# Optimization experiments

Measured on AMD Instinct MI355X. Metric: run time of the kernel, lower is better.

## Reference

```python
import jax, jax.numpy as jnp
import numpy as np

B, S, E, R = 128, 16, 512, 1000
_SCALE = np.float32(1.0 / np.sqrt(E))


def setup_inputs() -> dict:
    key = jax.random.key(0)
    ks = jax.random.split(key, 12)
    s = 1.0 / np.sqrt(E)
    u = lambda k, shape: jax.random.uniform(k, shape, jnp.float32, -s, s)
    emb = jax.random.normal(ks[0], (R + 1, E), jnp.float32).at[R].set(0.0)  # padding_idx row = 0
    return {
        "tokens": jax.random.randint(ks[11], (B, S), 0, R),
        "emb": emb,
        "W_ih": u(ks[1], (3 * E, E)), "W_hh": u(ks[2], (3 * E, E)),
        "b_ih": u(ks[3], (3 * E,)), "b_hh": u(ks[4], (3 * E,)),
        "w_fc": u(ks[5], (E,)), "b_fc": u(ks[6], ()),
        "Wq": u(ks[7], (E, E)), "bq": u(ks[8], (E,)),
        "Wk": u(ks[9], (E, E)), "bk": u(ks[10], (E,)),
    }


def _gru_step(x, h, W_ih, W_hh, b_ih, b_hh):
    # torch GRU cell: gates stacked as [r; z; n]
    gi = x @ W_ih.T + b_ih
    gh = h @ W_hh.T + b_hh
    ir, iz, inn = jnp.split(gi, 3, axis=-1)
    hr, hz, hn = jnp.split(gh, 3, axis=-1)
    r = jax.nn.sigmoid(ir + hr)
    z = jax.nn.sigmoid(iz + hz)
    n = jnp.tanh(inn + r * hn)
    return (1.0 - z) * n + z * h


def _attention(x, emb, Wq, bq, Wk, bk):
    # x: [B,1,E]; key = fc_k(cat(relation_emb, x)); scores = q k^T / sqrt(E)
    Bn = x.shape[0]
    rel = jnp.broadcast_to(emb[:R][None], (Bn, R, E))
    all_emb = jnp.concatenate([rel, x], axis=1)        # [B,R+1,E]
    q = x @ Wq.T + bq
    k = all_emb @ Wk.T + bk
    scores = jnp.einsum('bqe,bke->bqk', q, k) * _SCALE  # [B,1,R+1]
    return scores, all_emb


def _entropy(scores):
    lp = jax.nn.log_softmax(scores, axis=-1)
    return -jnp.sum(jnp.exp(lp) * lp, axis=-1)          # [B,1]


def _reduce(x, emb, W_ih, W_hh, b_ih, b_hh, w_fc, b_fc, Wq, bq, Wk, bk):
    Bn, L, Ed = x.shape
    if L > 2:
        # vectorized 2-step GRU over all adjacent pairs (replaces python while loop)
        h1 = _gru_step(x[:, :-1], jnp.zeros_like(x[:, :-1]), W_ih, W_hh, b_ih, b_hh)
        pairs = _gru_step(x[:, 1:], h1, W_ih, W_hh, b_ih, b_hh)   # [B,L-1,E]
        score = jax.nn.sigmoid(pairs @ w_fc + b_fc)               # [B,L-1]
        sel = jnp.argmax(score, axis=-1)                          # [B]
        barange = jnp.arange(Bn)
        pair = pairs[barange, sel][:, None]                       # [B,1,E]
        scores, all_emb = _attention(pair, emb, Wq, bq, Wk, bk)
        loss = _entropy(scores)
        prob = jax.nn.softmax(scores, axis=-1)                    # weightedAverage mask is all-False for seq_len=1
        merged = jnp.einsum('bqk,bke->bqe', prob, all_emb)[:, 0]  # [B,E]
        # output = inputs.detach().clone(); overwrite sel with merged; delete row sel+1
        out = jax.lax.stop_gradient(x).at[barange, sel].set(merged)
        j = jnp.arange(L - 1)[None]
        src = j + (j >= (sel + 1)[:, None])                       # skip zeroed row sel+1
        out = out[barange[:, None], src]                          # [B,L-1,E]
        return out, loss
    else:
        h1 = _gru_step(x[:, 0], jnp.zeros_like(x[:, 0]), W_ih, W_hh, b_ih, b_hh)
        h2 = _gru_step(x[:, 1], h1, W_ih, W_hh, b_ih, b_hh)
        return h2[:, None], jnp.zeros((Bn, 1), x.dtype)


def reference(tokens, emb, W_ih, W_hh, b_ih, b_hh, w_fc, b_fc, Wq, bq, Wk, bk):
    x = emb[tokens]                                               # [B,S,E]
    losses = []
    for _ in range(tokens.shape[1] - 1):
        x, l = _reduce(x, emb, W_ih, W_hh, b_ih, b_hh, w_fc, b_fc, Wq, bq, Wk, bk)
        losses.append(l)
    scores, _ = _attention(x, emb, Wq, bq, Wk, bk)                # x is [B,1,E]
    losses.append(_entropy(scores))
    return scores[:, 0], jnp.concatenate(losses, axis=-1)         # ([B,R+1], [B,S])
```

## Files before the change

### kernel.cpp

```cpp
#include <hip/hip_runtime.h>

#define B 128
#define S 16
#define E 512
#define R 1000
#define K3 1536
#define NW0 1920
#define NWS 256
#define NS (B * (R + 1))
#define SCALE 0.04419417382415922f

static __device__ __forceinline__ float sigm(float x) { return 1.f / (1.f + expf(-x)); }

static __device__ __forceinline__ float brsum(float v, float* sb) {
  int tid = threadIdx.x;
  sb[tid] = v; __syncthreads();
  for (int s = 128; s > 0; s >>= 1) {
    if (tid < s) sb[tid] += sb[tid + s];
    __syncthreads();
  }
  float r = sb[0]; __syncthreads();
  return r;
}
static __device__ __forceinline__ float brmax(float v, float* sb) {
  int tid = threadIdx.x;
  sb[tid] = v; __syncthreads();
  for (int s = 128; s > 0; s >>= 1) {
    if (tid < s) sb[tid] = fmaxf(sb[tid], sb[tid + s]);
    __syncthreads();
  }
  float r = sb[0]; __syncthreads();
  return r;
}
static __device__ __forceinline__ void brsum2(float v1, float v2, float* sb, float* sb2,
                                              float* o1, float* o2) {
  int tid = threadIdx.x;
  sb[tid] = v1; sb2[tid] = v2; __syncthreads();
  for (int s = 128; s > 0; s >>= 1) {
    if (tid < s) { sb[tid] += sb[tid + s]; sb2[tid] += sb2[tid + s]; }
    __syncthreads();
  }
  *o1 = sb[0]; *o2 = sb2[0]; __syncthreads();
}

#define TILE_FMA \
  _Pragma("unroll") \
  for (int k = 0; k < 16; ++k) { \
    float4 a4 = *(const float4*)&As[k][ty * 4]; \
    float4 w4 = *(const float4*)&Ws[k][tx * 4]; \
    acc[0][0] = fmaf(a4.x, w4.x, acc[0][0]); acc[0][1] = fmaf(a4.x, w4.y, acc[0][1]); \
    acc[0][2] = fmaf(a4.x, w4.z, acc[0][2]); acc[0][3] = fmaf(a4.x, w4.w, acc[0][3]); \
    acc[1][0] = fmaf(a4.y, w4.x, acc[1][0]); acc[1][1] = fmaf(a4.y, w4.y, acc[1][1]); \
    acc[1][2] = fmaf(a4.y, w4.z, acc[1][2]); acc[1][3] = fmaf(a4.y, w4.w, acc[1][3]); \
    acc[2][0] = fmaf(a4.z, w4.x, acc[2][0]); acc[2][1] = fmaf(a4.z, w4.y, acc[2][1]); \
    acc[2][2] = fmaf(a4.z, w4.z, acc[2][2]); acc[2][3] = fmaf(a4.z, w4.w, acc[2][3]); \
    acc[3][0] = fmaf(a4.w, w4.x, acc[3][0]); acc[3][1] = fmaf(a4.w, w4.y, acc[3][1]); \
    acc[3][2] = fmaf(a4.w, w4.z, acc[3][2]); acc[3][3] = fmaf(a4.w, w4.w, acc[3][3]); \
  }

#define TILE_FMA32 \
  _Pragma("unroll") \
  for (int k = 0; k < 16; ++k) { \
    float2 a2 = *(const float2*)&As[k][ty * 2]; \
    float4 w4 = *(const float4*)&Ws[k][tx * 4]; \
    acc[0][0] = fmaf(a2.x, w4.x, acc[0][0]); acc[0][1] = fmaf(a2.x, w4.y, acc[0][1]); \
    acc[0][2] = fmaf(a2.x, w4.z, acc[0][2]); acc[0][3] = fmaf(a2.x, w4.w, acc[0][3]); \
    acc[1][0] = fmaf(a2.y, w4.x, acc[1][0]); acc[1][1] = fmaf(a2.y, w4.y, acc[1][1]); \
    acc[1][2] = fmaf(a2.y, w4.z, acc[1][2]); acc[1][3] = fmaf(a2.y, w4.w, acc[1][3]); \
  }

__global__ __launch_bounds__(256) void k_gemm(const float* __restrict__ A, int lda, int M,
                                              const float* __restrict__ W, int N, int K,
                                              const float* __restrict__ bias, float scale,
                                              float* __restrict__ C, int ldc) {
  __shared__ float As[16][64];
  __shared__ float Ws[16][64];
  int tid = threadIdx.x;
  int mBase = blockIdx.y * 64;
  int nBase = blockIdx.x * 64;
  int tx = tid & 15, ty = tid >> 4;
  int li = tid & 63;
  int lk = (tid >> 6) * 4;
  float acc[4][4] = {{0.f,0.f,0.f,0.f},{0.f,0.f,0.f,0.f},{0.f,0.f,0.f,0.f},{0.f,0.f,0.f,0.f}};
  int m = mBase + li;
  const float* Arow = (m < M) ? (A + (size_t)m * lda) : nullptr;
  int n = nBase + li;
  const float* Wrow = (n < N) ? (W + (size_t)n * K) : nullptr;

  float4 av = Arow ? *(const float4*)(Arow + lk) : make_float4(0.f, 0.f, 0.f, 0.f);
  float4 wv = Wrow ? *(const float4*)(Wrow + lk) : make_float4(0.f, 0.f, 0.f, 0.f);

  for (int k0 = 0; k0 < K; k0 += 16) {
    As[lk + 0][li] = av.x; As[lk + 1][li] = av.y;
    As[lk + 2][li] = av.z; As[lk + 3][li] = av.w;
    Ws[lk + 0][li] = wv.x; Ws[lk + 1][li] = wv.y;
    Ws[lk + 2][li] = wv.z; Ws[lk + 3][li] = wv.w;
    __syncthreads();
    if (k0 + 16 < K) {
      av = Arow ? *(const float4*)(Arow + k0 + 16 + lk) : make_float4(0.f, 0.f, 0.f, 0.f);
      wv = Wrow ? *(const float4*)(Wrow + k0 + 16 + lk) : make_float4(0.f, 0.f, 0.f, 0.f);
    }
    TILE_FMA
    __syncthreads();
  }
#pragma unroll
  for (int r = 0; r < 4; ++r) {
    int mm = mBase + ty * 4 + r;
    if (mm >= M) continue;
#pragma unroll
    for (int c = 0; c < 4; ++c) {
      int nn = nBase + tx * 4 + c;
      if (nn >= N) continue;
      float v = acc[r][c] * scale;
      if (bias) v += bias[nn];
      C[(size_t)mm * ldc + nn] = v;
    }
  }
}

__global__ __launch_bounds__(256) void k_gemmD(const float* __restrict__ A, int lda, int M,
                                               const float* __restrict__ W1, int N1,
                                               const float* __restrict__ b1,
                                               float* __restrict__ C1, int ldc1,
                                               const float* __restrict__ W2, int N2,
                                               float* __restrict__ C2, int ldc2, int K) {
  __shared__ float As[16][64];
  __shared__ float Ws[16][64];
  int tid = threadIdx.x;
  int mBase = blockIdx.y * 64;
  int nBase = blockIdx.x * 64;
  int tx = tid & 15, ty = tid >> 4;
  int li = tid & 63;
  int lk = (tid >> 6) * 4;
  float acc[4][4] = {{0.f,0.f,0.f,0.f},{0.f,0.f,0.f,0.f},{0.f,0.f,0.f,0.f},{0.f,0.f,0.f,0.f}};
  int m = mBase + li;
  const float* Arow = (m < M) ? (A + (size_t)m * lda) : nullptr;
  int n = nBase + li;
  const float* Wrow = nullptr;
  if (n < N1) Wrow = W1 + (size_t)n * K;
  else if (n < N1 + N2) Wrow = W2 + (size_t)(n - N1) * K;

  float4 av = Arow ? *(const float4*)(Arow + lk) : make_float4(0.f, 0.f, 0.f, 0.f);
  float4 wv = Wrow ? *(const float4*)(Wrow + lk) : make_float4(0.f, 0.f, 0.f, 0.f);

  for (int k0 = 0; k0 < K; k0 += 16) {
    As[lk + 0][li] = av.x; As[lk + 1][li] = av.y;
    As[lk + 2][li] = av.z; As[lk + 3][li] = av.w;
    Ws[lk + 0][li] = wv.x; Ws[lk + 1][li] = wv.y;
    Ws[lk + 2][li] = wv.z; Ws[lk + 3][li] = wv.w;
    __syncthreads();
    if (k0 + 16 < K) {
      av = Arow ? *(const float4*)(Arow + k0 + 16 + lk) : make_float4(0.f, 0.f, 0.f, 0.f);
      wv = Wrow ? *(const float4*)(Wrow + k0 + 16 + lk) : make_float4(0.f, 0.f, 0.f, 0.f);
    }
    TILE_FMA
    __syncthreads();
  }
#pragma unroll
  for (int r = 0; r < 4; ++r) {
    int mm = mBase + ty * 4 + r;
    if (mm >= M) continue;
#pragma unroll
    for (int c = 0; c < 4; ++c) {
      int nn = nBase + tx * 4 + c;
      if (nn < N1) {
        float v = acc[r][c];
        if (b1) v += b1[nn];
        C1[(size_t)mm * ldc1 + nn] = v;
      } else if (nn < N1 + N2) {
        C2[(size_t)mm * ldc2 + (nn - N1)] = acc[r][c];
      }
    }
  }
}

static __device__ void dev_g64(float (*As)[64], float (*Ws)[64], int tid,
                               int mBase, int nBase,
                               const float* __restrict__ A, int lda, int M,
                               const float* __restrict__ W, int N, int K,
                               const float* __restrict__ bias, float scale,
                               float* __restrict__ C, int ldc) {
  int tx = tid & 15, ty = tid >> 4;
  int li = tid & 63;
  int lk = (tid >> 6) * 4;
  float acc[4][4] = {{0.f,0.f,0.f,0.f},{0.f,0.f,0.f,0.f},{0.f,0.f,0.f,0.f},{0.f,0.f,0.f,0.f}};
  int m = mBase + li;
  const float* Arow = (m < M) ? (A + (size_t)m * lda) : nullptr;
  int n = nBase + li;
  const float* Wrow = (n < N) ? (W + (size_t)n * K) : nullptr;

  float4 av = Arow ? *(const float4*)(Arow + lk) : make_float4(0.f, 0.f, 0.f, 0.f);
  float4 wv = Wrow ? *(const float4*)(Wrow + lk) : make_float4(0.f, 0.f, 0.f, 0.f);

  for (int k0 = 0; k0 < K; k0 += 16) {
    As[lk + 0][li] = av.x; As[lk + 1][li] = av.y;
    As[lk + 2][li] = av.z; As[lk + 3][li] = av.w;
    Ws[lk + 0][li] = wv.x; Ws[lk + 1][li] = wv.y;
    Ws[lk + 2][li] = wv.z; Ws[lk + 3][li] = wv.w;
    __syncthreads();
    if (k0 + 16 < K) {
      av = Arow ? *(const float4*)(Arow + k0 + 16 + lk) : make_float4(0.f, 0.f, 0.f, 0.f);
      wv = Wrow ? *(const float4*)(Wrow + k0 + 16 + lk) : make_float4(0.f, 0.f, 0.f, 0.f);
    }
    TILE_FMA
    __syncthreads();
  }
#pragma unroll
  for (int r = 0; r < 4; ++r) {
    int mm = mBase + ty * 4 + r;
    if (mm >= M) continue;
#pragma unroll
    for (int c = 0; c < 4; ++c) {
      int nn = nBase + tx * 4 + c;
      if (nn >= N) continue;
      float v = acc[r][c] * scale;
      if (bias) v += bias[nn];
      C[(size_t)mm * ldc + nn] = v;
    }
  }
}

static __device__ void dev_tr64(float (*t)[65], int tid, const float* __restrict__ src,
                                int Cc, float* __restrict__ dst, int ldd, int bx, int by) {
  int tx = tid & 15, ty = tid >> 4;
  int rb = by * 64, cb = bx * 64;
#pragma unroll
  for (int i = 0; i < 4; ++i) {
    int r = rb + ty + i * 16;
    float4 v = *(const float4*)(src + (size_t)r * Cc + cb + tx * 4);
    t[ty + i * 16][tx * 4 + 0] = v.x; t[ty + i * 16][tx * 4 + 1] = v.y;
    t[ty + i * 16][tx * 4 + 2] = v.z; t[ty + i * 16][tx * 4 + 3] = v.w;
  }
  __syncthreads();
#pragma unroll
  for (int i = 0; i < 4; ++i) {
    int c = cb + ty + i * 16;
    float4 v;
    v.x = t[tx * 4 + 0][ty + i * 16]; v.y = t[tx * 4 + 1][ty + i * 16];
    v.z = t[tx * 4 + 2][ty + i * 16]; v.w = t[tx * 4 + 3][ty + i * 16];
    *(float4*)(dst + (size_t)c * ldd + rb + tx * 4) = v;
  }
}

__global__ __launch_bounds__(256) void k_prep(const float* __restrict__ Wq,
                                              const float* __restrict__ Wk,
                                              const float* __restrict__ Wih,
                                              float* __restrict__ WqT,
                                              float* __restrict__ WkT,
                                              float* __restrict__ Wbig,
                                              int* __restrict__ pos,
                                              int* __restrict__ wlb,
                                              int* __restrict__ wlL,
                                              int* __restrict__ wlR,
                                              float* __restrict__ outp) {
  __shared__ float t[64][65];
  int blk = blockIdx.x, tid = threadIdx.x;
  if (blk < 64) {
    dev_tr64(t, tid, Wq, E, WqT, E, blk & 7, blk >> 3);
  } else if (blk < 128) {
    int j = blk - 64;
    dev_tr64(t, tid, Wk, E, WkT, E, j & 7, j >> 3);
  } else if (blk < 320) {
    int j = blk - 128;
    dev_tr64(t, tid, Wih, E, Wbig + (size_t)1024 * K3, K3, j & 7, j >> 3);
  } else if (blk < 328) {
    int idx = (blk - 320) * 256 + tid;
    if (idx < B * 16) pos[idx] = idx & 15;
    if (idx < NW0) {
      wlb[idx] = idx / 15;
      int i = idx % 15;
      wlL[idx] = i;
      wlR[idx] = i + 1;
    }
    if (idx < B) outp[NS + idx * 16 + 14] = 0.f;
  } else {
    int idx = (blk - 328) * 256 + tid;
    for (int i = idx; i < 24 * K3; i += 8 * 256) Wbig[(size_t)1000 * K3 + i] = 0.f;
  }
}

__global__ __launch_bounds__(256) void k_setup3(const float* __restrict__ KREL,
                                                const float* __restrict__ WqT,
                                                const float* __restrict__ WkT,
                                                const float* __restrict__ bq,
                                                const float* __restrict__ bk,
                                                float* __restrict__ Gbig,
                                                float* __restrict__ v12,
                                                float* __restrict__ c0s,
                                                float* __restrict__ gb) {
  __shared__ float As[16][64];
  __shared__ float Ws[16][64];
  int blk = blockIdx.x, tid = threadIdx.x;
  if (blk < 128) {
    dev_g64(As, Ws, tid, (blk >> 3) * 64, (blk & 7) * 64, KREL, E, R, WqT, E, E,
            nullptr, 1.f, Gbig, E);
  } else if (blk < 192) {
    int j = blk - 128;
    dev_g64(As, Ws, tid, (j >> 3) * 64, (j & 7) * 64, WqT, E, E, WkT, E, E,
            nullptr, 1.f, Gbig + (size_t)1000 * E, E);
  } else {
    int m = blk - 192;
    if (m < 2) {
      int i = m * 256 + tid;
      const float* wq = WqT + (size_t)i * E;
      const float* wk = WkT + (size_t)i * E;
      float s = 0.f;
      for (int e = 0; e < E; ++e) s += wq[e] * bk[e] + bq[e] * wk[e];
      v12[i] = s;
    } else if (m == 2) {
      float* sb = (float*)As;
      float p = 0.f;
      for (int e = tid; e < E; e += 256) p += bq[e] * bk[e];
      float s = brsum(p, sb);
      if (tid == 0) c0s[0] = s;
    } else {
      int r = (m - 3) * 256 + tid;
      if (r < R) {
        const float* kr = KREL + (size_t)r * E;
        float s = 0.f;
        for (int e = 0; e < E; ++e) s += bq[e] * kr[e];
        gb[r] = s;
      }
    }
  }
}

__global__ __launch_bounds__(256) void k_giinit(const int* __restrict__ tokens,
                                                const float* __restrict__ Wbig,
                                                const float* __restrict__ bih,
                                                float* __restrict__ GI,
                                                const float* __restrict__ gb,
                                                float* __restrict__ SCT,
                                                const float* __restrict__ bhh,
                                                float* __restrict__ H1C) {
  int row = blockIdx.x, tid = threadIdx.x;
  if (row < B * S) {
    int tok = tokens[row];
    const float4* src = (const float4*)(Wbig + (size_t)tok * K3);
    const float4* bv = (const float4*)bih;
    float* girow = GI + (size_t)row * K3;
    float4* dst = (float4*)girow;
    for (int i = tid; i < K3 / 4; i += 256) {
      float4 a = src[i], b = bv[i];
      dst[i] = make_float4(a.x + b.x, a.y + b.y, a.z + b.z, a.w + b.w);
    }
    int i16 = row & 15;
    if (i16 < 15) {
      __syncthreads();
      float* h = H1C + (size_t)((row >> 4) * 15 + i16) * E;
      for (int e = tid; e < E; e += 256) {
        float r = sigm(girow[e] + bhh[e]);
        float z = sigm(girow[E + e] + bhh[E + e]);
        h[e] = (1.f - z) * tanhf(girow[2 * E + e] + r * bhh[2 * E + e]);
      }
    }
  } else {
    int rb = row - B * S;
    for (int m = rb * 16; m < rb * 16 + 16; ++m) {
      float* r = SCT + (size_t)m * K3;
      for (int n = tid; n < 1512; n += 256) r[n] = (n < 1000) ? gb[n] : 0.f;
    }
  }
}

__global__ __launch_bounds__(256) void k_h1c(const int* __restrict__ wlb,
                                             const int* __restrict__ wlL,
                                             const float* __restrict__ GI,
                                             const float* __restrict__ bhh,
                                             float* __restrict__ H1C,
                                             float* __restrict__ GHC) {
  int w = blockIdx.x, tid = threadIdx.x;
  const float* gi = GI + (size_t)(wlb[w] * 16 + wlL[w]) * K3;
  float* h = H1C + (size_t)w * E;
  for (int e = tid; e < E; e += 256) {
    float r = sigm(gi[e] + bhh[e]);
    float z = sigm(gi[E + e] + bhh[E + e]);
    h[e] = (1.f - z) * tanhf(gi[2 * E + e] + r * bhh[2 * E + e]);
  }
  if (GHC) {
    float* g = GHC + (size_t)w * K3;
    for (int n = tid; n < K3; n += 256) g[n] = bhh[n];
  }
}

__global__ __launch_bounds__(256) void k_ghcs(const float* __restrict__ H1C,
                                              const float* __restrict__ Whh,
                                              float* __restrict__ GHC) {
  __shared__ float As[16][32];
  __shared__ float Ws[16][64];
  int tid = threadIdx.x;
  int nBase = blockIdx.x * 64;
  int mBase = blockIdx.y * 32;
  int kbeg = blockIdx.z * 256;
  int tx = tid & 15, ty = tid >> 4;
  int ar = tid & 31, ak = (tid >> 5) * 2;
  int li = tid & 63, lk = (tid >> 6) * 4;
  float acc[2][4] = {{0.f,0.f,0.f,0.f},{0.f,0.f,0.f,0.f}};
  const float* Arow = H1C + (size_t)(mBase + ar) * E + kbeg;
  const float* Wrow = Whh + (size_t)(nBase + li) * E + kbeg;
  float2 av = *(const float2*)(Arow + ak);
  float4 wv = *(const float4*)(Wrow + lk);
  for (int k0 = 0; k0 < 256; k0 += 16) {
    As[ak + 0][ar] = av.x; As[ak + 1][ar] = av.y;
    Ws[lk + 0][li] = wv.x; Ws[lk + 1][li] = wv.y;
    Ws[lk + 2][li] = wv.z; Ws[lk + 3][li] = wv.w;
    __syncthreads();
    if (k0 + 16 < 256) {
      av = *(const float2*)(Arow + k0 + 16 + ak);
      wv = *(const float4*)(Wrow + k0 + 16 + lk);
    }
    TILE_FMA32
    __syncthreads();
  }
#pragma unroll
  for (int r = 0; r < 2; ++r) {
    int mm = mBase + ty * 2 + r;
#pragma unroll
    for (int c = 0; c < 4; ++c) {
      int nn = nBase + tx * 4 + c;
      atomicAdd(&GHC[(size_t)mm * K3 + nn], acc[r][c]);
    }
  }
}

__global__ __launch_bounds__(256) void k_pairc(const int* __restrict__ wlb,
                                               const int* __restrict__ wlL,
                                               const int* __restrict__ wlR,
                                               const float* __restrict__ GI,
                                               const float* __restrict__ GHC,
                                               const float* __restrict__ H1C,
                                               const float* __restrict__ wfc,
                                               const float* __restrict__ bfc,
                                               float* __restrict__ PAIR,
                                               float* __restrict__ SCR) {
  __shared__ float sb[256];
  int w = blockIdx.x, tid = threadIdx.x;
  int b = wlb[w], ls = wlL[w], rs = wlR[w];
  const float* gr = GI + (size_t)(b * 16 + rs) * K3;
  const float* gh = GHC + (size_t)w * K3;
  const float* h = H1C + (size_t)w * E;
  float* p = PAIR + (size_t)(b * 16 + ls) * E;
  float part = 0.f;
  for (int e = tid; e < E; e += 256) {
    float r = sigm(gr[e] + gh[e]);
    float z = sigm(gr[E + e] + gh[E + e]);
    float n = tanhf(gr[2 * E + e] + r * gh[2 * E + e]);
    float pv = (1.f - z) * n + z * h[e];
    p[e] = pv;
    part += pv * wfc[e];
  }
  float d = brsum(part, sb);
  if (tid == 0) SCR[b * 16 + ls] = sigm(d + bfc[0]);
}

__global__ __launch_bounds__(256) void k_qscsel(const float* __restrict__ PAIR,
                                                const float* __restrict__ SCR,
                                                const int* __restrict__ pin,
                                                int* __restrict__ pout,
                                                int* __restrict__ wlb,
                                                int* __restrict__ wlL,
                                                int* __restrict__ wlR,
                                                int* __restrict__ xdst,
                                                const float* __restrict__ Gbig,
                                                float* __restrict__ SCT,
                                                float* __restrict__ GI,
                                                const float* __restrict__ bih,
                                                int P, int finalMode) {
  __shared__ float As[16][32];
  __shared__ float Ws[16][64];
  __shared__ int sxd[32];
  int tid = threadIdx.x;
  int nBase = blockIdx.x * 64;
  int mBase = blockIdx.y * 32;
  int kbeg = blockIdx.z * 256;
  if (tid < 32) {
    int b = mBase + tid;
    if (finalMode) {
      int xr = b * 16 + pin[b * 16];
      sxd[tid] = xr;
      if (blockIdx.x == 0 && blockIdx.z == 0) xdst[b] = xr;
    } else {
      int L = P + 1;
      int lp[16];
      for (int i = 0; i < L; ++i) lp[i] = pin[b * 16 + i];
      float best = -1e30f; int sel = 0;
      for (int i = 0; i < P; ++i) {
        float v = SCR[b * 16 + lp[i]];
        if (v > best) { best = v; sel = i; }
      }
      int r1i = (sel + 2 < L) ? sel + 2 : L - 1;
      int l1 = lp[sel], r1 = lp[r1i];
      int l0 = (sel > 0) ? lp[sel - 1] : l1;
      int r0 = (sel > 0) ? lp[sel] : r1;
      sxd[tid] = b * 16 + l1;
      if (blockIdx.x == 0 && blockIdx.z == 0) {
        wlb[2 * b] = b;     wlL[2 * b] = l0;     wlR[2 * b] = r0;
        wlb[2 * b + 1] = b; wlL[2 * b + 1] = l1; wlR[2 * b + 1] = r1;
        xdst[b] = b * 16 + l1;
        for (int i = 0; i < L - 1; ++i)
          pout[b * 16 + i] = (i <= sel) ? lp[i] : lp[i + 1];
      }
    }
  }
  __syncthreads();
  if (!finalMode && blockIdx.z == 1 && blockIdx.x < 16) {
#pragma unroll
    for (int r = 0; r < 2; ++r) {
      float* g = GI + (size_t)sxd[blockIdx.x * 2 + r] * K3;
      for (int i = tid; i < K3; i += 256) g[i] = bih[i];
    }
  }
  int tx = tid & 15, ty = tid >> 4;
  int ar = tid & 31, ak = (tid >> 5) * 2;
  int li = tid & 63, lk = (tid >> 6) * 4;
  float acc[2][4] = {{0.f,0.f,0.f,0.f},{0.f,0.f,0.f,0.f}};
  const float* Arow = PAIR + (size_t)sxd[ar] * E + kbeg;
  int n = nBase + li;
  const float* Wrow = (n < 1512) ? (Gbig + (size_t)n * E + kbeg) : nullptr;
  float2 av = *(const float2*)(Arow + ak);
  float4 wv = Wrow ? *(const float4*)(Wrow + lk) : make_float4(0.f, 0.f, 0.f, 0.f);
  for (int k0 = 0; k0 < 256; k0 += 16) {
    As[ak + 0][ar] = av.x; As[ak + 1][ar] = av.y;
    Ws[lk + 0][li] = wv.x; Ws[lk + 1][li] = wv.y;
    Ws[lk + 2][li] = wv.z; Ws[lk + 3][li] = wv.w;
    __syncthreads();
    if (k0 + 16 < 256) {
      av = *(const float2*)(Arow + k0 + 16 + ak);
      wv = Wrow ? *(const float4*)(Wrow + k0 + 16 + lk) : make_float4(0.f, 0.f, 0.f, 0.f);
    }
    TILE_FMA32
    __syncthreads();
  }
#pragma unroll
  for (int r = 0; r < 2; ++r) {
    int mm = mBase + ty * 2 + r;
#pragma unroll
    for (int c = 0; c < 4; ++c) {
      int nn = nBase + tx * 4 + c;
      if (nn < 1512) atomicAdd(&SCT[(size_t)mm * K3 + nn], acc[r][c]);
    }
  }
}

__global__ __launch_bounds__(256) void k_sm(float* __restrict__ SCT,
                                            const float* __restrict__ PAIR,
                                            const int* __restrict__ xdst,
                                            const float* __restrict__ v12,
                                            const float* __restrict__ c0s,
                                            float* __restrict__ outp,
                                            float* __restrict__ A2,
                                            const float* __restrict__ gb,
                                            int t, int finalMode) {
  __shared__ float sb[256];
  __shared__ float sb2[256];
  __shared__ float sps[E];
  int b = blockIdx.x, tid = threadIdx.x;
  float* row = SCT + (size_t)b * K3;
  int xr = xdst[b];
  const float* sp = PAIR + (size_t)xr * E;
  for (int i = tid; i < E; i += 256) sps[i] = sp[i];
  __syncthreads();
  float part = 0.f;
  for (int i = tid; i < E; i += 256) part += sps[i] * (row[1000 + i] + v12[i]);
  float last = (brsum(part, sb) + c0s[0]) * SCALE;
  float s[4];
  float ml = last;
#pragma unroll
  for (int q = 0; q < 4; ++q) {
    int j = tid + q * 256;
    s[q] = (j < 1000) ? row[j] * SCALE : -1e30f;
    ml = fmaxf(ml, s[q]);
  }
  float mx = brmax(ml, sb);
  float zp = 0.f, s1p = 0.f;
#pragma unroll
  for (int q = 0; q < 4; ++q) {
    int j = tid + q * 256;
    if (j < 1000) { float e = expf(s[q] - mx); zp += e; s1p += e * s[q]; }
  }
  if (tid == 0) { float e = expf(last - mx); zp += e; s1p += e * last; }
  float z, s1;
  brsum2(zp, s1p, sb, sb2, &z, &s1);
  if (tid == 0) outp[NS + b * 16 + t] = mx + logf(z) - s1 / z;
  if (!finalMode) {
    float inv = 1.f / z;
    float* a = A2 + (size_t)b * K3;
#pragma unroll
    for (int q = 0; q < 4; ++q) {
      int j = tid + q * 256;
      if (j < 1000) a[j] = expf(s[q] - mx) * inv;
    }
    if (tid < 24) a[1000 + tid] = 0.f;
    float pr = expf(last - mx) * inv;
    for (int i = tid; i < E; i += 256) a[1024 + i] = pr * sps[i];
    for (int n2 = tid; n2 < 1512; n2 += 256) row[n2] = (n2 < 1000) ? gb[n2] : 0.f;
  } else {
    float* so = outp + (size_t)b * (R + 1);
#pragma unroll
    for (int q = 0; q < 4; ++q) {
      int j = tid + q * 256;
      if (j < 1000) so[j] = s[q];
    }
    if (tid == 0) so[R] = last;
  }
}

__global__ __launch_bounds__(256) void k_giup(const float* __restrict__ A2,
                                              const float* __restrict__ Wbig,
                                              float* __restrict__ GI,
                                              const int* __restrict__ xdst) {
  __shared__ float As[16][32];
  __shared__ float Ws[16][64];
  int tid = threadIdx.x;
  int nBase = blockIdx.x * 64;
  int mBase = blockIdx.y * 32;
  int kbeg = blockIdx.z * 384;
  int tx = tid & 15, ty = tid >> 4;
  int ar = tid & 31, ak = (tid >> 5) * 2;
  int li = tid & 63, wr = tid >> 6;
  float acc[2][4] = {{0.f,0.f,0.f,0.f},{0.f,0.f,0.f,0.f}};
  const float* Arow = A2 + (size_t)(mBase + ar) * K3;
  for (int k0 = kbeg; k0 < kbeg + 384; k0 += 16) {
    float2 av = *(const float2*)(Arow + k0 + ak);
    As[ak + 0][ar] = av.x; As[ak + 1][ar] = av.y;
#pragma unroll
    for (int j = 0; j < 4; ++j)
      Ws[wr * 4 + j][li] = Wbig[(size_t)(k0 + wr * 4 + j) * K3 + nBase + li];
    __syncthreads();
    TILE_FMA32
    __syncthreads();
  }
#pragma unroll
  for (int r = 0; r < 2; ++r) {
    int mm = mBase + ty * 2 + r;
    size_t crow = (size_t)xdst[mm] * K3;
#pragma unroll
    for (int c = 0; c < 4; ++c) {
      int nn = nBase + tx * 4 + c;
      atomicAdd(&GI[crow + nn], acc[r][c]);
    }
  }
}

extern "C" void kernel_launch(void* const* d_in, const int* in_sizes, int n_in,
                              void* d_out, int out_size, void* d_ws, size_t ws_size,
                              hipStream_t stream) {
  (void)in_sizes; (void)n_in; (void)out_size; (void)ws_size;
  const int* tokens = (const int*)d_in[0];
  const float* emb = (const float*)d_in[1];
  const float* W_ih = (const float*)d_in[2];
  const float* W_hh = (const float*)d_in[3];
  const float* b_ih = (const float*)d_in[4];
  const float* b_hh = (const float*)d_in[5];
  const float* w_fc = (const float*)d_in[6];
  const float* b_fc = (const float*)d_in[7];
  const float* Wq = (const float*)d_in[8];
  const float* bq = (const float*)d_in[9];
  const float* Wk = (const float*)d_in[10];
  const float* bk = (const float*)d_in[11];
  float* out = (float*)d_out;

  float* ws = (float*)d_ws;
  size_t o = 0;
  float* GI = ws + o;    o += (size_t)B * S * K3;
  float* GHC = ws + o;   o += (size_t)NW0 * K3;
  float* H1C = ws + o;   o += (size_t)NW0 * E;
  float* PAIR = ws + o;  o += (size_t)B * S * E;
  float* Wbig = ws + o;  o += (size_t)K3 * K3;
  float* Gbig = ws + o;  o += (size_t)1512 * E;
  float* KREL = ws + o;  o += (size_t)R * E;
  float* WqT = ws + o;   o += (size_t)E * E;
  float* WkT = ws + o;   o += (size_t)E * E;
  float* SCT = ws + o;   o += (size_t)B * K3;
  float* A2 = ws + o;    o += (size_t)B * K3;
  float* gb = ws + o;    o += 1024;
  float* v12 = ws + o;   o += 512;
  float* c0s = ws + o;   o += 16;
  float* SCR = ws + o;   o += B * 16;
  int* pos0 = (int*)(ws + o); o += B * 16;
  int* pos1 = (int*)(ws + o); o += B * 16;
  int* wlb = (int*)(ws + o);  o += NW0;
  int* wlL = (int*)(ws + o);  o += NW0;
  int* wlR = (int*)(ws + o);  o += NW0;
  int* xdst = (int*)(ws + o); o += B;

  k_prep<<<336, 256, 0, stream>>>(Wq, Wk, W_ih, WqT, WkT, Wbig, pos0, wlb, wlL, wlR, out);
  k_gemmD<<<dim3(32, 16), 256, 0, stream>>>(emb, E, R, Wk, E, bk, KREL, E,
                                            W_ih, K3, Wbig, K3, E);
  k_setup3<<<199, 256, 0, stream>>>(KREL, WqT, WkT, bq, bk, Gbig, v12, c0s, gb);
  k_giinit<<<B * S + 8, 256, 0, stream>>>(tokens, Wbig, b_ih, GI, gb, SCT, b_hh, H1C);
  k_gemm<<<dim3(24, 30), 256, 0, stream>>>(H1C, E, NW0, W_hh, K3, E, b_hh, 1.f, GHC, K3);
  k_pairc<<<NW0, 256, 0, stream>>>(wlb, wlL, wlR, GI, GHC, H1C, w_fc, b_fc, PAIR, SCR);

  for (int t = 0; t < 14; ++t) {
    int* pin = (t & 1) ? pos1 : pos0;
    int* pout = (t & 1) ? pos0 : pos1;
    k_qscsel<<<dim3(24, 4, 2), 256, 0, stream>>>(PAIR, SCR, pin, pout, wlb, wlL, wlR,
                                                 xdst, Gbig, SCT, GI, b_ih, 15 - t, 0);
    k_sm<<<B, 256, 0, stream>>>(SCT, PAIR, xdst, v12, c0s, out, A2, gb, t, 0);
    k_giup<<<dim3(24, 4, 4), 256, 0, stream>>>(A2, Wbig, GI, xdst);
    k_h1c<<<NWS, 256, 0, stream>>>(wlb, wlL, GI, b_hh, H1C, GHC);
    k_ghcs<<<dim3(24, 8, 2), 256, 0, stream>>>(H1C, W_hh, GHC);
    k_pairc<<<NWS, 256, 0, stream>>>(wlb, wlL, wlR, GI, GHC, H1C, w_fc, b_fc, PAIR, SCR);
  }

  k_qscsel<<<dim3(24, 4, 2), 256, 0, stream>>>(PAIR, SCR, pos0, pos1, wlb, wlL, wlR,
                                               xdst, Gbig, SCT, GI, b_ih, 1, 1);
  k_sm<<<B, 256, 0, stream>>>(SCT, PAIR, xdst, v12, c0s, out, A2, gb, 15, 1);
}
```

Measured before the change: 1.450 ms.

## Cache GRU first-step state per position and recompute only merged rows

The first-step hidden state and its W_hh product are now stored per token position instead of per worklist pair entry. Each iteration recomputes only the one merged position per batch (B rows) rather than every affected pair (NWS rows), which halves the ghcs grid. The GI-init kernel is fused into the setup kernel, and the gb bias is added inside k_sm instead of being pre-filled into SCT. This trades slightly larger workspace buffers and an indirect row lookup for less recompute and one fewer launch.

Result: faster. 1.358 ms (-6.3%).

```diff
diff --git a/kernel.cpp b/kernel.cpp
--- a/kernel.cpp
+++ b/kernel.cpp
@@ -287,7 +287,14 @@
                                                 float* __restrict__ Gbig,
                                                 float* __restrict__ v12,
                                                 float* __restrict__ c0s,
-                                                float* __restrict__ gb) {
+                                                float* __restrict__ gb,
+                                                const int* __restrict__ tokens,
+                                                const float* __restrict__ Wbig,
+                                                const float* __restrict__ bih,
+                                                const float* __restrict__ bhh,
+                                                float* __restrict__ GI,
+                                                float* __restrict__ H1P,
+                                                float* __restrict__ SCT) {
   __shared__ float As[16][64];
   __shared__ float Ws[16][64];
   int blk = blockIdx.x, tid = threadIdx.x;
@@ -298,7 +305,7 @@
     int j = blk - 128;
     dev_g64(As, Ws, tid, (j >> 3) * 64, (j & 7) * 64, WqT, E, E, WkT, E, E,
             nullptr, 1.f, Gbig + (size_t)1000 * E, E);
-  } else {
+  } else if (blk < 199) {
     int m = blk - 192;
     if (m < 2) {
       int i = m * 256 + tid;
@@ -322,19 +329,8 @@
         gb[r] = s;
       }
     }
-  }
-}
-
-__global__ __launch_bounds__(256) void k_giinit(const int* __restrict__ tokens,
-                                                const float* __restrict__ Wbig,
-                                                const float* __restrict__ bih,
-                                                float* __restrict__ GI,
-                                                const float* __restrict__ gb,
-                                                float* __restrict__ SCT,
-                                                const float* __restrict__ bhh,
-                                                float* __restrict__ H1C) {
-  int row = blockIdx.x, tid = threadIdx.x;
-  if (row < B * S) {
+  } else if (blk < 199 + B * S) {
+    int row = blk - 199;
     int tok = tokens[row];
     const float4* src = (const float4*)(Wbig + (size_t)tok * K3);
     const float4* bv = (const float4*)bih;
@@ -344,59 +340,57 @@
       float4 a = src[i], b = bv[i];
       dst[i] = make_float4(a.x + b.x, a.y + b.y, a.z + b.z, a.w + b.w);
     }
-    int i16 = row & 15;
-    if (i16 < 15) {
-      __syncthreads();
-      float* h = H1C + (size_t)((row >> 4) * 15 + i16) * E;
-      for (int e = tid; e < E; e += 256) {
-        float r = sigm(girow[e] + bhh[e]);
-        float z = sigm(girow[E + e] + bhh[E + e]);
-        h[e] = (1.f - z) * tanhf(girow[2 * E + e] + r * bhh[2 * E + e]);
-      }
+    __syncthreads();
+    float* h = H1P + (size_t)row * E;
+    for (int e = tid; e < E; e += 256) {
+      float r = sigm(girow[e] + bhh[e]);
+      float z = sigm(girow[E + e] + bhh[E + e]);
+      h[e] = (1.f - z) * tanhf(girow[2 * E + e] + r * bhh[2 * E + e]);
     }
   } else {
-    int rb = row - B * S;
+    int rb = blk - (199 + B * S);
     for (int m = rb * 16; m < rb * 16 + 16; ++m) {
       float* r = SCT + (size_t)m * K3;
-      for (int n = tid; n < 1512; n += 256) r[n] = (n < 1000) ? gb[n] : 0.f;
-    }
-  }
-}
-
-__global__ __launch_bounds__(256) void k_h1c(const int* __restrict__ wlb,
-                                             const int* __restrict__ wlL,
+      for (int n = tid; n < 1512; n += 256) r[n] = 0.f;
+    }
+  }
+}
+
+__global__ __launch_bounds__(256) void k_h1c(const int* __restrict__ xdst,
                                              const float* __restrict__ GI,
                                              const float* __restrict__ bhh,
-                                             float* __restrict__ H1C,
-                                             float* __restrict__ GHC) {
-  int w = blockIdx.x, tid = threadIdx.x;
-  const float* gi = GI + (size_t)(wlb[w] * 16 + wlL[w]) * K3;
-  float* h = H1C + (size_t)w * E;
+                                             float* __restrict__ H1P,
+                                             float* __restrict__ GHCP) {
+  int p = xdst[blockIdx.x], tid = threadIdx.x;
+  const float* gi = GI + (size_t)p * K3;
+  float* h = H1P + (size_t)p * E;
   for (int e = tid; e < E; e += 256) {
     float r = sigm(gi[e] + bhh[e]);
     float z = sigm(gi[E + e] + bhh[E + e]);
     h[e] = (1.f - z) * tanhf(gi[2 * E + e] + r * bhh[2 * E + e]);
   }
-  if (GHC) {
-    float* g = GHC + (size_t)w * K3;
-    for (int n = tid; n < K3; n += 256) g[n] = bhh[n];
-  }
-}
-
-__global__ __launch_bounds__(256) void k_ghcs(const float* __restrict__ H1C,
+  float* g = GHCP + (size_t)p * K3;
+  for (int n = tid; n < K3; n += 256) g[n] = bhh[n];
+}
+
+__global__ __launch_bounds__(256) void k_ghcs(const int* __restrict__ xdst,
+                                              const float* __restrict__ H1P,
                                               const float* __restrict__ Whh,
-                                              float* __restrict__ GHC) {
+                                              float* __restrict__ GHCP) {
   __shared__ float As[16][32];
   __shared__ float Ws[16][64];
+  __shared__ int sp[32];
   int tid = threadIdx.x;
   int nBase = blockIdx.x * 64;
   int mBase = blockIdx.y * 32;
   int kbeg = blockIdx.z * 256;
+  if (tid < 32) sp[tid] = xdst[mBase + tid];
+  __syncthreads();
   int tx = tid & 15, ty = tid >> 4;
   int ar = tid & 31, ak = (tid >> 5) * 2;
   int li = tid & 63, lk = (tid >> 6) * 4;
   float acc[2][4] = {{0.f,0.f,0.f,0.f},{0.f,0.f,0.f,0.f}};
-  const float* Arow = H1C + (size_t)(mBase + ar) * E + kbeg;
+  const float* Arow = H1P + (size_t)sp[ar] * E + kbeg;
   const float* Wrow = Whh + (size_t)(nBase + li) * E + kbeg;
   float2 av = *(const float2*)(Arow + ak);
   float4 wv = *(const float4*)(Wrow + lk);
@@ -414,11 +408,11 @@
   }
 #pragma unroll
   for (int r = 0; r < 2; ++r) {
-    int mm = mBase + ty * 2 + r;
+    size_t crow = (size_t)sp[ty * 2 + r] * K3;
 #pragma unroll
     for (int c = 0; c < 4; ++c) {
       int nn = nBase + tx * 4 + c;
-      atomicAdd(&GHC[(size_t)mm * K3 + nn], acc[r][c]);
+      atomicAdd(&GHCP[crow + nn], acc[r][c]);
     }
   }
 }
@@ -427,8 +421,8 @@
                                                const int* __restrict__ wlL,
                                                const int* __restrict__ wlR,
                                                const float* __restrict__ GI,
-                                               const float* __restrict__ GHC,
-                                               const float* __restrict__ H1C,
+                                               const float* __restrict__ GHCP,
+                                               const float* __restrict__ H1P,
                                                const float* __restrict__ wfc,
                                                const float* __restrict__ bfc,
                                                float* __restrict__ PAIR,
@@ -436,10 +430,11 @@
   __shared__ float sb[256];
   int w = blockIdx.x, tid = threadIdx.x;
   int b = wlb[w], ls = wlL[w], rs = wlR[w];
+  int lp = b * 16 + ls;
   const float* gr = GI + (size_t)(b * 16 + rs) * K3;
-  const float* gh = GHC + (size_t)w * K3;
-  const float* h = H1C + (size_t)w * E;
-  float* p = PAIR + (size_t)(b * 16 + ls) * E;
+  const float* gh = GHCP + (size_t)lp * K3;
+  const float* h = H1P + (size_t)lp * E;
+  float* p = PAIR + (size_t)lp * E;
   float part = 0.f;
   for (int e = tid; e < E; e += 256) {
     float r = sigm(gr[e] + gh[e]);
@@ -568,7 +563,7 @@
 #pragma unroll
   for (int q = 0; q < 4; ++q) {
     int j = tid + q * 256;
-    s[q] = (j < 1000) ? row[j] * SCALE : -1e30f;
+    s[q] = (j < 1000) ? (row[j] + gb[j]) * SCALE : -1e30f;
     ml = fmaxf(ml, s[q]);
   }
   float mx = brmax(ml, sb);
@@ -593,7 +588,7 @@
     if (tid < 24) a[1000 + tid] = 0.f;
     float pr = expf(last - mx) * inv;
     for (int i = tid; i < E; i += 256) a[1024 + i] = pr * sps[i];
-    for (int n2 = tid; n2 < 1512; n2 += 256) row[n2] = (n2 < 1000) ? gb[n2] : 0.f;
+    for (int n2 = tid; n2 < 1512; n2 += 256) row[n2] = 0.f;
   } else {
     float* so = outp + (size_t)b * (R + 1);
 #pragma unroll
@@ -663,8 +658,8 @@
   float* ws = (float*)d_ws;
   size_t o = 0;
   float* GI = ws + o;    o += (size_t)B * S * K3;
-  float* GHC = ws + o;   o += (size_t)NW0 * K3;
-  float* H1C = ws + o;   o += (size_t)NW0 * E;
+  float* GHCP = ws + o;  o += (size_t)B * S * K3;
+  float* H1P = ws + o;   o += (size_t)B * S * E;
   float* PAIR = ws + o;  o += (size_t)B * S * E;
   float* Wbig = ws + o;  o += (size_t)K3 * K3;
   float* Gbig = ws + o;  o += (size_t)1512 * E;
@@ -687,10 +682,11 @@
   k_prep<<<336, 256, 0, stream>>>(Wq, Wk, W_ih, WqT, WkT, Wbig, pos0, wlb, wlL, wlR, out);
   k_gemmD<<<dim3(32, 16), 256, 0, stream>>>(emb, E, R, Wk, E, bk, KREL, E,
                                             W_ih, K3, Wbig, K3, E);
-  k_setup3<<<199, 256, 0, stream>>>(KREL, WqT, WkT, bq, bk, Gbig, v12, c0s, gb);
-  k_giinit<<<B * S + 8, 256, 0, stream>>>(tokens, Wbig, b_ih, GI, gb, SCT, b_hh, H1C);
-  k_gemm<<<dim3(24, 30), 256, 0, stream>>>(H1C, E, NW0, W_hh, K3, E, b_hh, 1.f, GHC, K3);
-  k_pairc<<<NW0, 256, 0, stream>>>(wlb, wlL, wlR, GI, GHC, H1C, w_fc, b_fc, PAIR, SCR);
+  k_setup3<<<199 + B * S + 8, 256, 0, stream>>>(KREL, WqT, WkT, bq, bk, Gbig, v12, c0s,
+                                                gb, tokens, Wbig, b_ih, b_hh, GI, H1P, SCT);
+  k_gemm<<<dim3(24, 32), 256, 0, stream>>>(H1P, E, B * S, W_hh, K3, E, b_hh, 1.f,
+                                           GHCP, K3);
+  k_pairc<<<NW0, 256, 0, stream>>>(wlb, wlL, wlR, GI, GHCP, H1P, w_fc, b_fc, PAIR, SCR);
 
   for (int t = 0; t < 14; ++t) {
     int* pin = (t & 1) ? pos1 : pos0;
@@ -699,9 +695,9 @@
                                                  xdst, Gbig, SCT, GI, b_ih, 15 - t, 0);
     k_sm<<<B, 256, 0, stream>>>(SCT, PAIR, xdst, v12, c0s, out, A2, gb, t, 0);
     k_giup<<<dim3(24, 4, 4), 256, 0, stream>>>(A2, Wbig, GI, xdst);
-    k_h1c<<<NWS, 256, 0, stream>>>(wlb, wlL, GI, b_hh, H1C, GHC);
-    k_ghcs<<<dim3(24, 8, 2), 256, 0, stream>>>(H1C, W_hh, GHC);
-    k_pairc<<<NWS, 256, 0, stream>>>(wlb, wlL, wlR, GI, GHC, H1C, w_fc, b_fc, PAIR, SCR);
+    k_h1c<<<B, 256, 0, stream>>>(xdst, GI, b_hh, H1P, GHCP);
+    k_ghcs<<<dim3(24, 4, 2), 256, 0, stream>>>(xdst, H1P, W_hh, GHCP);
+    k_pairc<<<NWS, 256, 0, stream>>>(wlb, wlL, wlR, GI, GHCP, H1P, w_fc, b_fc, PAIR, SCR);
   }
 
   k_qscsel<<<dim3(24, 4, 2), 256, 0, stream>>>(PAIR, SCR, pos0, pos1, wlb, wlL, wlR,
```
